# Performance work log

Hardware: AMD Instinct MI355X
Metric: run time of the kernel (lower is better)

The kernel has to match this reference:

```python
import jax, jax.numpy as jnp
import numpy as np

EMB = 1280
MD = 200
N = 20000
E = 200000
LN_EPS = 1e-5


def _layer_norm(x, g, b):
    mu = jnp.mean(x, axis=-1, keepdims=True)
    var = jnp.mean((x - mu) ** 2, axis=-1, keepdims=True)
    return (x - mu) * jax.lax.rsqrt(var + LN_EPS) * g + b


def _gat_conv(x, edge_index, edge_attr, W, We, a_src, a_dst, a_edge, bias, heads, C):
    """PyG GATConv (bias-free lin, edge_dim, add_self_loops with fill='mean')."""
    n = x.shape[0]
    src, dst = edge_index[0], edge_index[1]
    # self-loop edge_attr = mean of incoming edge_attr per dst node (0 if none)
    cnt = jax.ops.segment_sum(jnp.ones((edge_attr.shape[0],), x.dtype), dst, n)
    s = jax.ops.segment_sum(edge_attr, dst, n)
    loop_attr = jnp.where(cnt[:, None] > 0, s / jnp.maximum(cnt, 1.0)[:, None], 0.0)
    loop = jnp.arange(n)
    src = jnp.concatenate([src, loop])
    dst = jnp.concatenate([dst, loop])
    ea = jnp.concatenate([edge_attr, loop_attr], axis=0)
    h = (x @ W).reshape(n, heads, C)                      # [N,H,C]
    al_s = jnp.einsum('nhc,hc->nh', h, a_src)
    al_d = jnp.einsum('nhc,hc->nh', h, a_dst)
    eh = (ea @ We).reshape(-1, heads, C)                  # [E+N,H,C]
    al_e = jnp.einsum('ehc,hc->eh', eh, a_edge)
    alpha = jax.nn.leaky_relu(al_s[src] + al_d[dst] + al_e, 0.2)
    amax = jax.ops.segment_max(alpha, dst, n)
    amax = jnp.where(jnp.isfinite(amax), amax, 0.0)
    ex = jnp.exp(alpha - amax[dst])
    denom = jax.ops.segment_sum(ex, dst, n)
    w = ex / (denom[dst] + 1e-16)                         # segment softmax over dst
    out = jax.ops.segment_sum(h[src] * w[:, :, None], dst, n)
    return out.reshape(n, heads * C) + bias


def _forward(x, edge_index, edge_attr,
             ca_qw, ca_qb, ca_kw, ca_kb, ca_vw, ca_vb, ca_ow, ca_ob,
             g0_w, g0_ew, g0_as, g0_ad, g0_ae, g0_b, ln0_g, ln0_b,
             g1_w, g1_ew, g1_as, g1_ad, g1_ae, g1_b, ln1_g, ln1_b,
             g2_w, g2_ew, g2_as, g2_ad, g2_ae, g2_b, ln2_g, ln2_b,
             cls_w1, cls_b1, cls_w2, cls_b2):
    xe = x[:, :EMB]
    md = x[0, EMB:]
    # CrossAttention: single md vector -> K,V are [1,hidden]
    Q = xe @ ca_qw + ca_qb                                # [N,hid]
    K = md @ ca_kw + ca_kb                                # [hid]
    V = md @ ca_vw + ca_vb                                # [hid]
    scores = (Q @ K) / jnp.sqrt(jnp.asarray(Q.shape[-1], Q.dtype))  # [N]
    wts = jax.nn.softmax(scores, axis=0)[:, None]         # softmax over nodes
    attended = wts * V[None, :]                           # [N,hid]
    h = attended @ ca_ow + ca_ob + xe                     # [N,EMB]

    h = _gat_conv(h, edge_index, edge_attr, g0_w, g0_ew, g0_as, g0_ad, g0_ae, g0_b, 4, 256)
    h = jax.nn.relu(_layer_norm(h, ln0_g, ln0_b))
    h = _gat_conv(h, edge_index, edge_attr, g1_w, g1_ew, g1_as, g1_ad, g1_ae, g1_b, 4, 256)
    h = jax.nn.relu(_layer_norm(h, ln1_g, ln1_b))
    h = _gat_conv(h, edge_index, edge_attr, g2_w, g2_ew, g2_as, g2_ad, g2_ae, g2_b, 1, 256)
    h = jax.nn.relu(_layer_norm(h, ln2_g, ln2_b))

    g = jnp.mean(h, axis=0, keepdims=True)                # [1,256]
    g = jax.nn.relu(g @ cls_w1 + cls_b1)
    return g @ cls_w2 + cls_b2                            # [1,2]


def setup_inputs() -> dict:
    key = jax.random.key(0)
    ks = jax.random.split(key, 64)
    i = [0]
    def nrm(shape, scale=0.05):
        i[0] += 1
        return jax.random.normal(ks[i[0]], shape, jnp.float32) * scale
    inp = {}
    inp['x'] = nrm((N, EMB + MD), 1.0)
    inp['edge_index'] = jax.random.randint(ks[60], (2, E), 0, N, jnp.int64 if jax.config.read('jax_enable_x64') else jnp.int32)
    inp['edge_attr'] = jax.random.uniform(ks[61], (E, 1), jnp.float32)
    inp.update(ca_qw=nrm((EMB, 256)), ca_qb=jnp.zeros((256,), jnp.float32),
               ca_kw=nrm((MD, 256)), ca_kb=jnp.zeros((256,), jnp.float32),
               ca_vw=nrm((MD, 256)), ca_vb=jnp.zeros((256,), jnp.float32),
               ca_ow=nrm((256, EMB)), ca_ob=jnp.zeros((EMB,), jnp.float32))
    inp.update(g0_w=nrm((EMB, 1024)), g0_ew=nrm((1, 1024)), g0_as=nrm((4, 256)),
               g0_ad=nrm((4, 256)), g0_ae=nrm((4, 256)), g0_b=jnp.zeros((1024,), jnp.float32),
               ln0_g=jnp.ones((1024,), jnp.float32), ln0_b=jnp.zeros((1024,), jnp.float32))
    inp.update(g1_w=nrm((1024, 1024)), g1_ew=nrm((1, 1024)), g1_as=nrm((4, 256)),
               g1_ad=nrm((4, 256)), g1_ae=nrm((4, 256)), g1_b=jnp.zeros((1024,), jnp.float32),
               ln1_g=jnp.ones((1024,), jnp.float32), ln1_b=jnp.zeros((1024,), jnp.float32))
    inp.update(g2_w=nrm((1024, 256)), g2_ew=nrm((1, 256)), g2_as=nrm((1, 256)),
               g2_ad=nrm((1, 256)), g2_ae=nrm((1, 256)), g2_b=jnp.zeros((256,), jnp.float32),
               ln2_g=jnp.ones((256,), jnp.float32), ln2_b=jnp.zeros((256,), jnp.float32))
    inp.update(cls_w1=nrm((256, 128)), cls_b1=jnp.zeros((128,), jnp.float32),
               cls_w2=nrm((128, 2)), cls_b2=jnp.zeros((2,), jnp.float32))
    return inp


def reference(x, edge_index, edge_attr,
              ca_qw, ca_qb, ca_kw, ca_kb, ca_vw, ca_vb, ca_ow, ca_ob,
              g0_w, g0_ew, g0_as, g0_ad, g0_ae, g0_b, ln0_g, ln0_b,
              g1_w, g1_ew, g1_as, g1_ad, g1_ae, g1_b, ln1_g, ln1_b,
              g2_w, g2_ew, g2_as, g2_ad, g2_ae, g2_b, ln2_g, ln2_b,
              cls_w1, cls_b1, cls_w2, cls_b2):
    return _forward(x, edge_index, edge_attr,
                    ca_qw, ca_qb, ca_kw, ca_kb, ca_vw, ca_vb, ca_ow, ca_ob,
                    g0_w, g0_ew, g0_as, g0_ad, g0_ae, g0_b, ln0_g, ln0_b,
                    g1_w, g1_ew, g1_as, g1_ad, g1_ae, g1_b, ln1_g, ln1_b,
                    g2_w, g2_ew, g2_as, g2_ad, g2_ae, g2_b, ln2_g, ln2_b,
                    cls_w1, cls_b1, cls_w2, cls_b2)
```

## Files before the change

### kernel.cpp

```cpp
#include <hip/hip_runtime.h>
#include <hip/hip_bf16.h>
#include <math.h>

#define N_NODES 20000
#define N_EDGES 200000
#define XROW    1480

typedef __attribute__((ext_vector_type(8))) _Float16 f16x8;
typedef __attribute__((ext_vector_type(8))) unsigned short u16x8;
typedef __attribute__((ext_vector_type(4))) float f32x4v;

__device__ __forceinline__ float wsum(float v){
#pragma unroll
  for (int o=32;o>0;o>>=1) v += __shfl_down(v,o);
  return v;
}
__device__ __forceinline__ float wmax(float v){
#pragma unroll
  for (int o=32;o>0;o>>=1) v = fmaxf(v,__shfl_down(v,o));
  return v;
}
__device__ __forceinline__ float wsum_all(float v){
#pragma unroll
  for (int o=32;o>0;o>>=1) v += __shfl_xor(v,o);
  return v;
}
__device__ __forceinline__ float wmax_all(float v){
#pragma unroll
  for (int o=32;o>0;o>>=1) v = fmaxf(v,__shfl_xor(v,o));
  return v;
}

__device__ __forceinline__ unsigned short f2hu(float f){
  _Float16 h = (_Float16)f;
  return __builtin_bit_cast(unsigned short, h);
}
__device__ __forceinline__ float hu2f(unsigned short u){
  return (float)__builtin_bit_cast(_Float16, u);
}

__device__ __forceinline__ void async_copy16(void* lds, const void* g){
  __builtin_amdgcn_global_load_lds((const __attribute__((address_space(1))) void*)g,
                                   (__attribute__((address_space(3))) void*)lds, 16, 0, 0);
}

__global__ void edge_count_kernel(const int* __restrict__ ei, const float* __restrict__ ea,
                                  int* __restrict__ cnt, float* __restrict__ easum, int E){
  int e = blockIdx.x*256 + threadIdx.x;
  if (e >= E) return;
  int dst = ei[E + e];
  atomicAdd(&cnt[dst], 1);
  atomicAdd(&easum[dst], ea[e]);
}

__launch_bounds__(1024)
__global__ void scan_kernel(const int* __restrict__ cnt, const float* __restrict__ easum,
                            int* __restrict__ off, float* __restrict__ loop_attr, int n){
  __shared__ int buf[1024];
  const int PER = (N_NODES + 1023)/1024;
  int t = threadIdx.x;
  int base = t*PER;
  int local[PER];
  int s = 0;
#pragma unroll
  for (int k=0;k<PER;k++){
    int i = base + k;
    int v = (i<n)? cnt[i] : 0;
    local[k] = v;
    s += v;
  }
  buf[t] = s;
  __syncthreads();
  for (int d2=1; d2<1024; d2<<=1){
    int tv = (t>=d2)? buf[t-d2] : 0;
    __syncthreads();
    buf[t] += tv;
    __syncthreads();
  }
  int run = buf[t] - s;
#pragma unroll
  for (int k=0;k<PER;k++){
    int i = base + k;
    if (i < n){
      off[i] = run;
      int v = local[k];
      loop_attr[i] = (v>0) ? easum[i]/(float)v : 0.f;
      run += v;
    }
  }
  if (t == 1023) off[n] = buf[1023];
}

__global__ void edge_fill_kernel(const int* __restrict__ ei, const float* __restrict__ ea,
                                 const int* __restrict__ off, int* __restrict__ fill,
                                 int* __restrict__ csr_src, float* __restrict__ csr_ea, int E){
  int e = blockIdx.x*256 + threadIdx.x;
  if (e >= E) return;
  int dst = ei[E + e];
  int pos = off[dst] + atomicAdd(&fill[dst], 1);
  csr_src[pos] = ei[e];
  csr_ea[pos]  = ea[e];
}

__global__ void x_to_f16(const float* __restrict__ x, unsigned short* __restrict__ xh){
  const int CH4 = 1280/4;
  long total = (long)N_NODES*CH4;
  for (long i = (long)blockIdx.x*256 + threadIdx.x; i < total; i += (long)gridDim.x*256){
    int row = (int)(i / CH4), c4 = (int)(i % CH4);
    float4 v = *(const float4*)(x + (size_t)row*XROW + c4*4);
    ushort4 o;
    o.x = f2hu(v.x); o.y = f2hu(v.y); o.z = f2hu(v.z); o.w = f2hu(v.w);
    *(ushort4*)(xh + (size_t)row*1280 + c4*4) = o;
  }
}

__global__ void wt_f16_kernel(const float* __restrict__ W, int K, int N,
                              unsigned short* __restrict__ Wt){
  __shared__ float tile[32][33];
  int k0 = blockIdx.x*32, n0 = blockIdx.y*32;
  int tx = threadIdx.x & 31, ty = threadIdx.x >> 5;
  for (int r=ty; r<32; r+=8) tile[r][tx] = W[(size_t)(k0+r)*N + n0+tx];
  __syncthreads();
  for (int r=ty; r<32; r+=8){
    float w = tile[tx][r];
    Wt[(size_t)(n0+r)*K + k0+tx] = f2hu(w);
  }
}

__global__ void kv_kernel(const float* __restrict__ x,
                          const float* __restrict__ kw, const float* __restrict__ kb,
                          const float* __restrict__ vw, const float* __restrict__ vb,
                          float* __restrict__ Kv, float* __restrict__ Vv){
  int j = threadIdx.x;
  float ka = kb[j], va = vb[j];
  for (int k=0;k<200;k++){
    float m = x[1280+k];
    ka = fmaf(m, kw[k*256+j], ka);
    va = fmaf(m, vw[k*256+j], va);
  }
  Kv[j]=ka; Vv[j]=va;
}

__global__ void qkvo_kernel(const float* __restrict__ qw, const float* __restrict__ ow,
                            const float* __restrict__ Kv, const float* __restrict__ Vv,
                            float* __restrict__ qK, float* __restrict__ Vo){
  int idx = blockIdx.x*256 + threadIdx.x;
  if (idx < 1280){
    float a=0;
    for (int j=0;j<256;j++) a = fmaf(qw[idx*256+j], Kv[j], a);
    qK[idx]=a;
  } else if (idx < 2560){
    int j = idx-1280;
    float a=0;
    for (int i=0;i<256;i++) a = fmaf(Vv[i], ow[(size_t)i*1280+j], a);
    Vo[j]=a;
  }
}

__global__ void obw_kernel(const float* __restrict__ ob, const float* __restrict__ Vo,
                           const float* __restrict__ W, float* __restrict__ obW, float* __restrict__ VoW){
  int j = blockIdx.x*256 + threadIdx.x;
  float a=0,b=0;
  for (int i=0;i<1280;i++){
    float w = W[(size_t)i*1024+j];
    a = fmaf(ob[i], w, a);
    b = fmaf(Vo[i], w, b);
  }
  obW[j]=a; VoW[j]=b;
}

__launch_bounds__(256)
__global__ void scores_kernel(const unsigned short* __restrict__ xh, const float* __restrict__ qK,
                              float* __restrict__ scores, int n){
  __shared__ float qs[1280];
  int t = threadIdx.x;
  for (int i=t;i<1280;i+=256) qs[i]=qK[i];
  __syncthreads();
  int wid = t>>6, lane = t&63;
  int node = blockIdx.x*4 + wid;
  if (node >= n) return;
  const u16x8* row = (const u16x8*)(xh + (size_t)node*1280);
  float acc = 0;
#pragma unroll
  for (int it=0; it<3; it++){
    int chunk = it*64 + lane;
    if (chunk < 160){
      u16x8 v = row[chunk];
#pragma unroll
      for (int k=0;k<8;k++) acc = fmaf(hu2f(v[k]), qs[chunk*8+k], acc);
    }
  }
  acc = wsum(acc);
  if (lane==0) scores[node] = acc;
}

__launch_bounds__(1024)
__global__ void softmax_nodes(const float* __restrict__ scores, float* __restrict__ wts, int n){
  __shared__ float red[16];
  int t = threadIdx.x, lane=t&63, wid=t>>6;
  float m = -INFINITY;
  for (int i=t;i<n;i+=1024) m = fmaxf(m, scores[i]);
  m = wmax(m);
  if (lane==0) red[wid]=m;
  __syncthreads();
  if (t==0){ float r=red[0]; for (int k=1;k<16;k++) r=fmaxf(r,red[k]); red[0]=r; }
  __syncthreads();
  float M = red[0];
  __syncthreads();
  float z=0;
  for (int i=t;i<n;i+=1024) z += expf((scores[i]-M)*(1.f/16.f));
  z = wsum(z);
  if (lane==0) red[wid]=z;
  __syncthreads();
  if (t==0){ float r=0; for (int k=0;k<16;k++) r+=red[k]; red[0]=r; }
  __syncthreads();
  float invZ = 1.f/red[0];
  for (int i=t;i<n;i+=1024) wts[i] = expf((scores[i]-M)*(1.f/16.f))*invZ;
}

__launch_bounds__(256)
__global__ void gemm_f16(const unsigned short* __restrict__ A,
                         const unsigned short* __restrict__ B,
                         unsigned short* __restrict__ C, int M, int N, int K,
                         const float* __restrict__ addCol,
                         const float* __restrict__ vCol,
                         const float* __restrict__ wRow,
                         const float* __restrict__ a_src,
                         const float* __restrict__ a_dst,
                         float* __restrict__ alsp,
                         float* __restrict__ aldp)
{
  __shared__ short lds[2*2*128*64];

  const int ntc = N >> 7;
  const int sh  = __popc(ntc - 1);
  const int g   = blockIdx.y >> sh;
  const int nt  = blockIdx.y & (ntc - 1);
  const int band = blockIdx.x + (g << 3);
  if (band * 128 >= M) return;

  const int t = threadIdx.x;
  const int w = t>>6, l = t&63;
  const int bm = band*128, bn = nt*128;
  const int wr = (w>>1)*64, wc = (w&1)*64;
  const int half = w & 1;

  f32x4v acc[4][4];
#pragma unroll
  for (int i=0;i<4;i++)
#pragma unroll
    for (int j=0;j<4;j++) acc[i][j] = (f32x4v){0.f,0.f,0.f,0.f};

  const unsigned short* Ap[4]; const unsigned short* Bp[4];
  int ldsOff[4];
#pragma unroll
  for (int q=0;q<4;q++){
    int p  = (w*4+q)*64 + l;
    int r  = p>>3, pc = p&7;
    int kc = (pc ^ (r&7))*8;
    int rowA = bm + r; if (rowA > M-1) rowA = M-1;
    Ap[q] = A + (size_t)rowA*K + kc;
    Bp[q] = B + (size_t)(bn+r)*K + kc;
    ldsOff[q] = (w*4+q)*64*8;
  }

  const int nsteps = K >> 6;

#pragma unroll
  for (int q=0;q<4;q++) async_copy16(lds + ldsOff[q],        Ap[q]);
#pragma unroll
  for (int q=0;q<4;q++) async_copy16(lds + 8192 + ldsOff[q], Bp[q]);

  const int q4 = l>>4, m16 = l&15;

  for (int ks0=0; ks0<nsteps; ++ks0){
    short* curb = lds + (ks0&1)*16384;

    if (ks0+1 < nsteps){
      short* nxt = lds + ((ks0+1)&1)*16384;
      const int k0n = (ks0+1)*64;
#pragma unroll
      for (int q=0;q<4;q++) async_copy16(nxt + ldsOff[q],        Ap[q] + k0n);
#pragma unroll
      for (int q=0;q<4;q++) async_copy16(nxt + 8192 + ldsOff[q], Bp[q] + k0n);
      asm volatile("s_waitcnt vmcnt(8)" ::: "memory");
    } else {
      asm volatile("s_waitcnt vmcnt(0)" ::: "memory");
    }
    __builtin_amdgcn_sched_barrier(0);
    __builtin_amdgcn_s_barrier();
    __builtin_amdgcn_sched_barrier(0);

    __builtin_amdgcn_s_setprio(1);
#pragma unroll
    for (int ks=0; ks<2; ks++){
      f16x8 af[4], bf[4];
      const int c = ks*4 + q4;
#pragma unroll
      for (int i=0;i<4;i++){
        int ra = wr + i*16 + m16;
        af[i] = *(const f16x8*)&curb[ra*64 + ((c ^ (ra&7))*8)];
        int rb = wc + i*16 + m16;
        bf[i] = *(const f16x8*)&curb[8192 + rb*64 + ((c ^ (rb&7))*8)];
      }
#pragma unroll
      for (int i=0;i<4;i++)
#pragma unroll
        for (int j=0;j<4;j++)
          acc[i][j] = __builtin_amdgcn_mfma_f32_16x16x32_f16(af[i], bf[j], acc[i][j], 0,0,0);
    }
    __builtin_amdgcn_s_setprio(0);
    __builtin_amdgcn_sched_barrier(0);
    __builtin_amdgcn_s_barrier();
    __builtin_amdgcn_sched_barrier(0);
  }

  float* sred = (float*)lds;
  float* dred = sred + 256;
  float asv[4], adv[4];
#pragma unroll
  for (int j=0;j<4;j++){
    int n = bn + wc + j*16 + m16;
    asv[j] = a_src[n];
    adv[j] = a_dst[n];
  }
#pragma unroll
  for (int i=0;i<4;i++){
#pragma unroll
    for (int r=0;r<4;r++){
      int rloc = wr + i*16 + q4*4 + r;
      int m = bm + rloc;
      float wrow = addCol ? wRow[m < M ? m : M-1] : 0.f;
      float vj[4];
#pragma unroll
      for (int j=0;j<4;j++){
        int n = bn + wc + j*16 + m16;
        float v = acc[i][j][r];
        if (addCol) v += addCol[n] + wrow*vCol[n];
        vj[j] = v;
      }
      if (m < M){
        unsigned short* crow = C + (size_t)m*N;
#pragma unroll
        for (int j=0;j<4;j++) crow[bn + wc + j*16 + m16] = f2hu(vj[j]);
      }
      float s = vj[0]*asv[0] + vj[1]*asv[1] + vj[2]*asv[2] + vj[3]*asv[3];
      float d = vj[0]*adv[0] + vj[1]*adv[1] + vj[2]*adv[2] + vj[3]*adv[3];
#pragma unroll
      for (int o=1;o<16;o<<=1){ s += __shfl_xor(s,o); d += __shfl_xor(d,o); }
      if (m16 == 0){
        sred[half*128 + rloc] = s;
        dred[half*128 + rloc] = d;
      }
    }
  }
  __syncthreads();
  if (t < 128){
    int m = bm + t;
    if (m < M){
      alsp[(size_t)nt*M + m] = sred[t] + sred[128+t];
      aldp[(size_t)nt*M + m] = dred[t] + dred[128+t];
    }
  }
}

__global__ void als_combine(const float* __restrict__ alsp, const float* __restrict__ aldp,
                            float* __restrict__ als, float* __restrict__ ald, int M, int H){
  int idx = blockIdx.x*256 + threadIdx.x;
  if (idx >= M*H) return;
  int m = idx / H, hh = idx - m*H;
  als[idx] = alsp[(size_t)(2*hh)*M + m] + alsp[(size_t)(2*hh+1)*M + m];
  ald[idx] = aldp[(size_t)(2*hh)*M + m] + aldp[(size_t)(2*hh+1)*M + m];
}

template<int H>
__global__ void we_kernel(const float* __restrict__ We, const float* __restrict__ a_edge,
                          float* __restrict__ we){
  int wid = threadIdx.x>>6, lane = threadIdx.x&63;
  if (wid < H){
    const float4* w4 = (const float4*)(We + wid*256);
    const float4* a4 = (const float4*)(a_edge + wid*256);
    float4 a = w4[lane], b = a4[lane];
    float v = a.x*b.x + a.y*b.y + a.z*b.z + a.w*b.w;
    v = wsum(v);
    if (lane==0) we[wid]=v;
  }
}

template<int H>
__launch_bounds__(256)
__global__ void gat_agg_ln_wave(const unsigned short* __restrict__ hmat,
                           const float* __restrict__ als, const float* __restrict__ ald,
                           const int* __restrict__ off, const int* __restrict__ csr_src,
                           const float* __restrict__ csr_ea, const float* __restrict__ loop_attr,
                           const float* __restrict__ we,
                           const float* __restrict__ bias,
                           const float* __restrict__ ln_g, const float* __restrict__ ln_b,
                           float* __restrict__ outf, unsigned short* __restrict__ outb, int n)
{
  constexpr int OUT = 256*H;
  constexpr int CPL = OUT/64;
  const int wv = threadIdx.x>>6, lane = threadIdx.x&63;
  const int i = blockIdx.x*4 + wv;
  __shared__ float wbuf_s[4][64*H];
  __shared__ int   sbuf_s[4][64];
  if (i >= n) return;
  float* wbuf = wbuf_s[wv];
  int*   sbuf = sbuf_s[wv];

  const int begin = off[i];
  const int deg   = off[i+1]-begin;
  const int S     = deg + 1;

  float aldi[H], wei[H];
#pragma unroll
  for (int hh=0;hh<H;hh++){ aldi[hh]=ald[(size_t)i*H+hh]; wei[hh]=we[hh]; }
  const float lea = loop_attr[i];

  const int head = (lane*CPL) >> 8;
  const int c0   = lane*CPL;
  float acc[CPL];
#pragma unroll
  for (int c=0;c<CPL;c++) acc[c]=0.f;

  if (S <= 64){
    int src = i; float ev = lea;
    if (lane < deg){ src = csr_src[begin+lane]; ev = csr_ea[begin+lane]; }
    const bool act = lane < S;
    float a[H];
#pragma unroll
    for (int hh=0;hh<H;hh++){
      float v = als[(size_t)src*H+hh] + aldi[hh] + ev*wei[hh];
      a[hh] = v>0.f ? v : 0.2f*v;
    }
#pragma unroll
    for (int hh=0;hh<H;hh++){
      float M = wmax_all(act ? a[hh] : -INFINITY);
      float e = act ? __expf(a[hh]-M) : 0.f;
      float Z = wsum_all(e);
      wbuf[lane*H+hh] = e / (Z + 1e-16f);
    }
    sbuf[lane] = src;
    for (int j=0;j<S;j++){
      int sj = sbuf[j];
      float wj = wbuf[j*H+head];
      const unsigned short* row = hmat + (size_t)sj*OUT + c0;
      if constexpr (CPL==16){
        u16x8 r0 = *(const u16x8*)(row);
        u16x8 r1 = *(const u16x8*)(row+8);
#pragma unroll
        for (int c=0;c<8;c++){
          acc[c]   = fmaf(wj, hu2f(r0[c]), acc[c]);
          acc[8+c] = fmaf(wj, hu2f(r1[c]), acc[8+c]);
        }
      } else {
        ushort4 r = *(const ushort4*)(row);
        acc[0]=fmaf(wj,hu2f(r.x),acc[0]); acc[1]=fmaf(wj,hu2f(r.y),acc[1]);
        acc[2]=fmaf(wj,hu2f(r.z),acc[2]); acc[3]=fmaf(wj,hu2f(r.w),acc[3]);
      }
    }
  } else {
    float rm[H];
#pragma unroll
    for (int hh=0;hh<H;hh++) rm[hh] = -INFINITY;
    for (int s=lane; s<S; s+=64){
      int src = (s<deg)? csr_src[begin+s] : i;
      float ev = (s<deg)? csr_ea[begin+s] : lea;
#pragma unroll
      for (int hh=0;hh<H;hh++){
        float v = als[(size_t)src*H+hh] + aldi[hh] + ev*wei[hh];
        v = v>0.f? v : 0.2f*v;
        rm[hh] = fmaxf(rm[hh], v);
      }
    }
    float M[H], es[H];
#pragma unroll
    for (int hh=0;hh<H;hh++){ M[hh]=wmax_all(rm[hh]); es[hh]=0.f; }
    for (int s=lane; s<S; s+=64){
      int src = (s<deg)? csr_src[begin+s] : i;
      float ev = (s<deg)? csr_ea[begin+s] : lea;
#pragma unroll
      for (int hh=0;hh<H;hh++){
        float v = als[(size_t)src*H+hh] + aldi[hh] + ev*wei[hh];
        v = v>0.f? v : 0.2f*v;
        es[hh] += __expf(v - M[hh]);
      }
    }
    float invZ[H];
#pragma unroll
    for (int hh=0;hh<H;hh++) invZ[hh] = 1.f/(wsum_all(es[hh]) + 1e-16f);
    for (int cb=0; cb<S; cb+=64){
      int m = min(64, S-cb);
      int s = cb + lane;
      if (s < S){
        int src = (s<deg)? csr_src[begin+s] : i;
        float ev = (s<deg)? csr_ea[begin+s] : lea;
        sbuf[lane] = src;
#pragma unroll
        for (int hh=0;hh<H;hh++){
          float v = als[(size_t)src*H+hh] + aldi[hh] + ev*wei[hh];
          v = v>0.f? v : 0.2f*v;
          wbuf[lane*H+hh] = __expf(v - M[hh]) * invZ[hh];
        }
      }
      for (int j=0;j<m;j++){
        int sj = sbuf[j];
        float wj = wbuf[j*H+head];
        const unsigned short* row = hmat + (size_t)sj*OUT + c0;
        if constexpr (CPL==16){
          u16x8 r0 = *(const u16x8*)(row);
          u16x8 r1 = *(const u16x8*)(row+8);
#pragma unroll
          for (int c=0;c<8;c++){
            acc[c]   = fmaf(wj, hu2f(r0[c]), acc[c]);
            acc[8+c] = fmaf(wj, hu2f(r1[c]), acc[8+c]);
          }
        } else {
          ushort4 r = *(const ushort4*)(row);
          acc[0]=fmaf(wj,hu2f(r.x),acc[0]); acc[1]=fmaf(wj,hu2f(r.y),acc[1]);
          acc[2]=fmaf(wj,hu2f(r.z),acc[2]); acc[3]=fmaf(wj,hu2f(r.w),acc[3]);
        }
      }
    }
  }

  float vals[CPL];
  float ls=0.f;
#pragma unroll
  for (int c=0;c<CPL;c+=4){
    float4 b4 = *(const float4*)(bias + c0 + c);
    vals[c]=acc[c]+b4.x; vals[c+1]=acc[c+1]+b4.y; vals[c+2]=acc[c+2]+b4.z; vals[c+3]=acc[c+3]+b4.w;
    ls += vals[c]+vals[c+1]+vals[c+2]+vals[c+3];
  }
  float mu = wsum_all(ls) * (1.f/OUT);
  float lv=0.f;
#pragma unroll
  for (int c=0;c<CPL;c++){ float d=vals[c]-mu; lv += d*d; }
  float inv = rsqrtf(wsum_all(lv)*(1.f/OUT) + 1e-5f);

  if (outb){
    if constexpr (CPL==16){
#pragma unroll
      for (int c=0;c<CPL;c+=8){
        u16x8 o;
#pragma unroll
        for (int k=0;k<8;k++){
          float g = ln_g[c0+c+k], b = ln_b[c0+c+k];
          o[k] = f2hu(fmaxf((vals[c+k]-mu)*inv*g + b, 0.f));
        }
        *(u16x8*)(outb + (size_t)i*OUT + c0 + c) = o;
      }
    } else {
      ushort4 o;
      o.x = f2hu(fmaxf((vals[0]-mu)*inv*ln_g[c0+0] + ln_b[c0+0], 0.f));
      o.y = f2hu(fmaxf((vals[1]-mu)*inv*ln_g[c0+1] + ln_b[c0+1], 0.f));
      o.z = f2hu(fmaxf((vals[2]-mu)*inv*ln_g[c0+2] + ln_b[c0+2], 0.f));
      o.w = f2hu(fmaxf((vals[3]-mu)*inv*ln_g[c0+3] + ln_b[c0+3], 0.f));
      *(ushort4*)(outb + (size_t)i*OUT + c0) = o;
    }
  } else {
#pragma unroll
    for (int c=0;c<CPL;c+=4){
      float4 g4 = *(const float4*)(ln_g + c0 + c);
      float4 b4 = *(const float4*)(ln_b + c0 + c);
      float4 o;
      o.x = fmaxf((vals[c+0]-mu)*inv*g4.x + b4.x, 0.f);
      o.y = fmaxf((vals[c+1]-mu)*inv*g4.y + b4.y, 0.f);
      o.z = fmaxf((vals[c+2]-mu)*inv*g4.z + b4.z, 0.f);
      o.w = fmaxf((vals[c+3]-mu)*inv*g4.w + b4.w, 0.f);
      *(float4*)(outf + (size_t)i*OUT + c0 + c) = o;
    }
  }
}

__global__ void colsum_kernel(const float* __restrict__ h2, float* __restrict__ gsum, int n){
  int c = threadIdx.x;
  float acc=0;
  for (int i=blockIdx.x;i<n;i+=gridDim.x) acc += h2[(size_t)i*256 + c];
  atomicAdd(&gsum[c], acc);
}

__launch_bounds__(128)
__global__ void cls_kernel(const float* __restrict__ gsum,
                           const float* __restrict__ w1, const float* __restrict__ b1,
                           const float* __restrict__ w2, const float* __restrict__ b2,
                           float* __restrict__ outp){
  __shared__ float g[256];
  __shared__ float hid[128];
  int t = threadIdx.x;
  g[t]     = gsum[t]    *(1.f/N_NODES);
  g[t+128] = gsum[t+128]*(1.f/N_NODES);
  __syncthreads();
  float a = b1[t];
  for (int c=0;c<256;c++) a = fmaf(g[c], w1[c*128+t], a);
  hid[t] = fmaxf(a, 0.f);
  __syncthreads();
  if (t<2){
    float o = b2[t];
    for (int j=0;j<128;j++) o = fmaf(hid[j], w2[j*2+t], o);
    outp[t] = o;
  }
}

extern "C" void kernel_launch(void* const* d_in, const int* in_sizes, int n_in,
                              void* d_out, int out_size, void* d_ws, size_t ws_size,
                              hipStream_t stream)
{
  const float* x      = (const float*)d_in[0];
  const int*   ei     = (const int*)  d_in[1];
  const float* ea     = (const float*)d_in[2];
  const float* ca_qw  = (const float*)d_in[3];
  const float* ca_kw  = (const float*)d_in[5];
  const float* ca_kb  = (const float*)d_in[6];
  const float* ca_vw  = (const float*)d_in[7];
  const float* ca_vb  = (const float*)d_in[8];
  const float* ca_ow  = (const float*)d_in[9];
  const float* ca_ob  = (const float*)d_in[10];
  const float* g0_w   = (const float*)d_in[11];
  const float* g0_ew  = (const float*)d_in[12];
  const float* g0_as  = (const float*)d_in[13];
  const float* g0_ad  = (const float*)d_in[14];
  const float* g0_ae  = (const float*)d_in[15];
  const float* g0_b   = (const float*)d_in[16];
  const float* ln0_g  = (const float*)d_in[17];
  const float* ln0_b  = (const float*)d_in[18];
  const float* g1_w   = (const float*)d_in[19];
  const float* g1_ew  = (const float*)d_in[20];
  const float* g1_as  = (const float*)d_in[21];
  const float* g1_ad  = (const float*)d_in[22];
  const float* g1_ae  = (const float*)d_in[23];
  const float* g1_b   = (const float*)d_in[24];
  const float* ln1_g  = (const float*)d_in[25];
  const float* ln1_b  = (const float*)d_in[26];
  const float* g2_w   = (const float*)d_in[27];
  const float* g2_ew  = (const float*)d_in[28];
  const float* g2_as  = (const float*)d_in[29];
  const float* g2_ad  = (const float*)d_in[30];
  const float* g2_ae  = (const float*)d_in[31];
  const float* g2_b   = (const float*)d_in[32];
  const float* ln2_g  = (const float*)d_in[33];
  const float* ln2_b  = (const float*)d_in[34];
  const float* cls_w1 = (const float*)d_in[35];
  const float* cls_b1 = (const float*)d_in[36];
  const float* cls_w2 = (const float*)d_in[37];
  const float* cls_b2 = (const float*)d_in[38];
  float* outp = (float*)d_out;

  const int N = N_NODES, E = N_EDGES;

  char* base = (char*)d_ws;
  size_t o = 0;
  auto alloc = [&](size_t bytes)->void*{
    void* p = base + o;
    o += (bytes + 255) & ~(size_t)255;
    return p;
  };
  unsigned short* hF   = (unsigned short*)alloc((size_t)N*1024*2);
  unsigned short* Af   = (unsigned short*)alloc((size_t)N*1280*2);
  float*          h2   = (float*)         alloc((size_t)N*256*4);
  unsigned short* Wt   = (unsigned short*)alloc((size_t)1280*1024*2);
  float* alsp      = (float*)alloc((size_t)8*N*4);
  float* aldp      = (float*)alloc((size_t)8*N*4);
  float* als       = (float*)alloc((size_t)2*N*4*4);
  float* ald       = als + (size_t)N*4;
  float* scores    = (float*)alloc((size_t)N*4);
  float* wts       = (float*)alloc((size_t)N*4);
  int*   cnt       = (int*)  alloc((size_t)N*4);
  float* easum     = (float*)alloc((size_t)N*4);
  int*   off       = (int*)  alloc((size_t)(N+1)*4);
  int*   fill      = (int*)  alloc((size_t)N*4);
  int*   csr_src   = (int*)  alloc((size_t)E*4);
  float* csr_ea    = (float*)alloc((size_t)E*4);
  float* loop_attr = (float*)alloc((size_t)N*4);
  float* Kv        = (float*)alloc(256*4);
  float* Vv        = (float*)alloc(256*4);
  float* qK        = (float*)alloc(1280*4);
  float* Vo        = (float*)alloc(1280*4);
  float* obW       = (float*)alloc(1024*4);
  float* VoW       = (float*)alloc(1024*4);
  float* web       = (float*)alloc(16*4);
  float* gsum      = (float*)alloc(256*4);

  hipMemsetAsync(cnt,   0, (size_t)N*4, stream);
  hipMemsetAsync(easum, 0, (size_t)N*4, stream);
  hipMemsetAsync(fill,  0, (size_t)N*4, stream);
  hipMemsetAsync(gsum,  0, 256*4,       stream);

  int eblocks = (E + 255)/256;
  edge_count_kernel<<<eblocks,256,0,stream>>>(ei, ea, cnt, easum, E);
  scan_kernel<<<1,1024,0,stream>>>(cnt, easum, off, loop_attr, N);
  edge_fill_kernel<<<eblocks,256,0,stream>>>(ei, ea, off, fill, csr_src, csr_ea, E);

  x_to_f16<<<2048,256,0,stream>>>(x, Af);

  kv_kernel<<<1,256,0,stream>>>(x, ca_kw, ca_kb, ca_vw, ca_vb, Kv, Vv);
  qkvo_kernel<<<10,256,0,stream>>>(ca_qw, ca_ow, Kv, Vv, qK, Vo);
  obw_kernel<<<4,256,0,stream>>>(ca_ob, Vo, g0_w, obW, VoW);
  scores_kernel<<<(N+3)/4,256,0,stream>>>(Af, qK, scores, N);
  softmax_nodes<<<1,1024,0,stream>>>(scores, wts, N);

  const int mTiles  = (N + 127)/128;
  const int mGroups = (mTiles + 7)/8;
  const int NB4 = (N + 3)/4;

  wt_f16_kernel<<<dim3(1280/32, 1024/32),256,0,stream>>>(g0_w, 1280, 1024, Wt);
  gemm_f16<<<dim3(8, mGroups*8),256,0,stream>>>(Af, Wt, hF, N, 1024, 1280, obW, VoW, wts,
                                                g0_as, g0_ad, alsp, aldp);
  als_combine<<<(N*4+255)/256,256,0,stream>>>(alsp, aldp, als, ald, N, 4);
  we_kernel<4><<<1,256,0,stream>>>(g0_ew, g0_ae, web);
  gat_agg_ln_wave<4><<<NB4,256,0,stream>>>(hF, als, ald, off, csr_src, csr_ea, loop_attr,
                                           web, g0_b, ln0_g, ln0_b, nullptr, Af, N);

  wt_f16_kernel<<<dim3(1024/32, 1024/32),256,0,stream>>>(g1_w, 1024, 1024, Wt);
  gemm_f16<<<dim3(8, mGroups*8),256,0,stream>>>(Af, Wt, hF, N, 1024, 1024, nullptr, nullptr, nullptr,
                                                g1_as, g1_ad, alsp, aldp);
  als_combine<<<(N*4+255)/256,256,0,stream>>>(alsp, aldp, als, ald, N, 4);
  we_kernel<4><<<1,256,0,stream>>>(g1_ew, g1_ae, web);
  gat_agg_ln_wave<4><<<NB4,256,0,stream>>>(hF, als, ald, off, csr_src, csr_ea, loop_attr,
                                           web, g1_b, ln1_g, ln1_b, nullptr, Af, N);

  wt_f16_kernel<<<dim3(1024/32, 256/32),256,0,stream>>>(g2_w, 1024, 256, Wt);
  gemm_f16<<<dim3(8, mGroups*2),256,0,stream>>>(Af, Wt, hF, N, 256, 1024, nullptr, nullptr, nullptr,
                                                g2_as, g2_ad, alsp, aldp);
  als_combine<<<(N+255)/256,256,0,stream>>>(alsp, aldp, als, ald, N, 1);
  we_kernel<1><<<1,256,0,stream>>>(g2_ew, g2_ae, web);
  gat_agg_ln_wave<1><<<NB4,256,0,stream>>>(hF, als, ald, off, csr_src, csr_ea, loop_attr,
                                           web, g2_b, ln2_g, ln2_b, h2, nullptr, N);

  colsum_kernel<<<256,256,0,stream>>>(h2, gsum, N);
  cls_kernel<<<1,128,0,stream>>>(gsum, cls_w1, cls_b1, cls_w2, cls_b2, outp);

  (void)in_sizes; (void)n_in; (void)out_size; (void)ws_size;
}
```

Before: 862.6 us.

## Fuse f16 conversion with scores, merge we into als_combine, prefetch gather rows

```diff
diff --git a/kernel.cpp b/kernel.cpp
--- a/kernel.cpp
+++ b/kernel.cpp
@@ -100,18 +100,6 @@
   int pos = off[dst] + atomicAdd(&fill[dst], 1);
   csr_src[pos] = ei[e];
   csr_ea[pos]  = ea[e];
-}
-
-__global__ void x_to_f16(const float* __restrict__ x, unsigned short* __restrict__ xh){
-  const int CH4 = 1280/4;
-  long total = (long)N_NODES*CH4;
-  for (long i = (long)blockIdx.x*256 + threadIdx.x; i < total; i += (long)gridDim.x*256){
-    int row = (int)(i / CH4), c4 = (int)(i % CH4);
-    float4 v = *(const float4*)(x + (size_t)row*XROW + c4*4);
-    ushort4 o;
-    o.x = f2hu(v.x); o.y = f2hu(v.y); o.z = f2hu(v.z); o.w = f2hu(v.w);
-    *(ushort4*)(xh + (size_t)row*1280 + c4*4) = o;
-  }
 }
 
 __global__ void wt_f16_kernel(const float* __restrict__ W, int K, int N,
@@ -170,8 +158,8 @@
 }
 
 __launch_bounds__(256)
-__global__ void scores_kernel(const unsigned short* __restrict__ xh, const float* __restrict__ qK,
-                              float* __restrict__ scores, int n){
+__global__ void xh_scores_kernel(const float* __restrict__ x, const float* __restrict__ qK,
+                                 unsigned short* __restrict__ xh, float* __restrict__ scores, int n){
   __shared__ float qs[1280];
   int t = threadIdx.x;
   for (int i=t;i<1280;i+=256) qs[i]=qK[i];
@@ -179,16 +167,20 @@
   int wid = t>>6, lane = t&63;
   int node = blockIdx.x*4 + wid;
   if (node >= n) return;
-  const u16x8* row = (const u16x8*)(xh + (size_t)node*1280);
-  float acc = 0;
-#pragma unroll
-  for (int it=0; it<3; it++){
-    int chunk = it*64 + lane;
-    if (chunk < 160){
-      u16x8 v = row[chunk];
-#pragma unroll
-      for (int k=0;k<8;k++) acc = fmaf(hu2f(v[k]), qs[chunk*8+k], acc);
-    }
+  const float* xr = x + (size_t)node*XROW;
+  unsigned short* orow = xh + (size_t)node*1280;
+  float acc = 0.f;
+#pragma unroll
+  for (int it=0; it<5; it++){
+    int c4 = it*64 + lane;
+    float4 v = *(const float4*)(xr + c4*4);
+    ushort4 o;
+    o.x = f2hu(v.x); o.y = f2hu(v.y); o.z = f2hu(v.z); o.w = f2hu(v.w);
+    *(ushort4*)(orow + c4*4) = o;
+    acc = fmaf(v.x, qs[c4*4+0], acc);
+    acc = fmaf(v.y, qs[c4*4+1], acc);
+    acc = fmaf(v.z, qs[c4*4+2], acc);
+    acc = fmaf(v.w, qs[c4*4+3], acc);
   }
   acc = wsum(acc);
   if (lane==0) scores[node] = acc;
@@ -208,14 +200,14 @@
   float M = red[0];
   __syncthreads();
   float z=0;
-  for (int i=t;i<n;i+=1024) z += expf((scores[i]-M)*(1.f/16.f));
+  for (int i=t;i<n;i+=1024) z += __expf((scores[i]-M)*(1.f/16.f));
   z = wsum(z);
   if (lane==0) red[wid]=z;
   __syncthreads();
   if (t==0){ float r=0; for (int k=0;k<16;k++) r+=red[k]; red[0]=r; }
   __syncthreads();
   float invZ = 1.f/red[0];
-  for (int i=t;i<n;i+=1024) wts[i] = expf((scores[i]-M)*(1.f/16.f))*invZ;
+  for (int i=t;i<n;i+=1024) wts[i] = __expf((scores[i]-M)*(1.f/16.f))*invZ;
 }
 
 __launch_bounds__(256)
@@ -365,26 +357,25 @@
 }
 
 __global__ void als_combine(const float* __restrict__ alsp, const float* __restrict__ aldp,
-                            float* __restrict__ als, float* __restrict__ ald, int M, int H){
+                            float* __restrict__ als, float* __restrict__ ald, int M, int H,
+                            const float* __restrict__ We, const float* __restrict__ a_edge,
+                            float* __restrict__ we){
+  if (blockIdx.x == 0){
+    int wid = threadIdx.x>>6, lane = threadIdx.x&63;
+    if (wid < H){
+      const float4* w4 = (const float4*)(We + wid*256);
+      const float4* a4 = (const float4*)(a_edge + wid*256);
+      float4 a = w4[lane], b = a4[lane];
+      float v = a.x*b.x + a.y*b.y + a.z*b.z + a.w*b.w;
+      v = wsum(v);
+      if (lane==0) we[wid]=v;
+    }
+  }
   int idx = blockIdx.x*256 + threadIdx.x;
   if (idx >= M*H) return;
   int m = idx / H, hh = idx - m*H;
   als[idx] = alsp[(size_t)(2*hh)*M + m] + alsp[(size_t)(2*hh+1)*M + m];
   ald[idx] = aldp[(size_t)(2*hh)*M + m] + aldp[(size_t)(2*hh+1)*M + m];
-}
-
-template<int H>
-__global__ void we_kernel(const float* __restrict__ We, const float* __restrict__ a_edge,
-                          float* __restrict__ we){
-  int wid = threadIdx.x>>6, lane = threadIdx.x&63;
-  if (wid < H){
-    const float4* w4 = (const float4*)(We + wid*256);
-    const float4* a4 = (const float4*)(a_edge + wid*256);
-    float4 a = w4[lane], b = a4[lane];
-    float v = a.x*b.x + a.y*b.y + a.z*b.z + a.w*b.w;
-    v = wsum(v);
-    if (lane==0) we[wid]=v;
-  }
 }
 
 template<int H>
@@ -427,36 +418,115 @@
     int src = i; float ev = lea;
     if (lane < deg){ src = csr_src[begin+lane]; ev = csr_ea[begin+lane]; }
     const bool act = lane < S;
-    float a[H];
-#pragma unroll
-    for (int hh=0;hh<H;hh++){
-      float v = als[(size_t)src*H+hh] + aldi[hh] + ev*wei[hh];
-      a[hh] = v>0.f ? v : 0.2f*v;
-    }
-#pragma unroll
-    for (int hh=0;hh<H;hh++){
-      float M = wmax_all(act ? a[hh] : -INFINITY);
-      float e = act ? __expf(a[hh]-M) : 0.f;
-      float Z = wsum_all(e);
-      wbuf[lane*H+hh] = e / (Z + 1e-16f);
-    }
     sbuf[lane] = src;
-    for (int j=0;j<S;j++){
-      int sj = sbuf[j];
-      float wj = wbuf[j*H+head];
-      const unsigned short* row = hmat + (size_t)sj*OUT + c0;
-      if constexpr (CPL==16){
-        u16x8 r0 = *(const u16x8*)(row);
-        u16x8 r1 = *(const u16x8*)(row+8);
+
+    if constexpr (CPL==16){
+      u16x8 a0r0,a0r1,a1r0,a1r1;
+      {
+        const unsigned short* r0p = hmat + (size_t)sbuf[0]*OUT + c0;
+        a0r0 = *(const u16x8*)r0p; a0r1 = *(const u16x8*)(r0p+8);
+        a1r0 = a0r0; a1r1 = a0r1;
+        if (S > 1){
+          const unsigned short* r1p = hmat + (size_t)sbuf[1]*OUT + c0;
+          a1r0 = *(const u16x8*)r1p; a1r1 = *(const u16x8*)(r1p+8);
+        }
+      }
+      float a[H];
+#pragma unroll
+      for (int hh=0;hh<H;hh++){
+        float v = als[(size_t)src*H+hh] + aldi[hh] + ev*wei[hh];
+        a[hh] = v>0.f ? v : 0.2f*v;
+      }
+#pragma unroll
+      for (int hh=0;hh<H;hh++){
+        float M = wmax_all(act ? a[hh] : -INFINITY);
+        float e = act ? __expf(a[hh]-M) : 0.f;
+        float Z = wsum_all(e);
+        wbuf[lane*H+hh] = e / (Z + 1e-16f);
+      }
+      int j = 0;
+      for (; j+2<S; j+=2){
+        u16x8 n0r0,n0r1,n1r0,n1r1;
+        {
+          const unsigned short* rp = hmat + (size_t)sbuf[j+2]*OUT + c0;
+          n0r0 = *(const u16x8*)rp; n0r1 = *(const u16x8*)(rp+8);
+          n1r0 = n0r0; n1r1 = n0r1;
+          if (j+3 < S){
+            const unsigned short* rq = hmat + (size_t)sbuf[j+3]*OUT + c0;
+            n1r0 = *(const u16x8*)rq; n1r1 = *(const u16x8*)(rq+8);
+          }
+        }
+        float w0 = wbuf[j*H+head], w1 = wbuf[(j+1)*H+head];
 #pragma unroll
         for (int c=0;c<8;c++){
-          acc[c]   = fmaf(wj, hu2f(r0[c]), acc[c]);
-          acc[8+c] = fmaf(wj, hu2f(r1[c]), acc[8+c]);
-        }
-      } else {
-        ushort4 r = *(const ushort4*)(row);
-        acc[0]=fmaf(wj,hu2f(r.x),acc[0]); acc[1]=fmaf(wj,hu2f(r.y),acc[1]);
-        acc[2]=fmaf(wj,hu2f(r.z),acc[2]); acc[3]=fmaf(wj,hu2f(r.w),acc[3]);
+          acc[c]   = fmaf(w0, hu2f(a0r0[c]), acc[c]);
+          acc[8+c] = fmaf(w0, hu2f(a0r1[c]), acc[8+c]);
+        }
+#pragma unroll
+        for (int c=0;c<8;c++){
+          acc[c]   = fmaf(w1, hu2f(a1r0[c]), acc[c]);
+          acc[8+c] = fmaf(w1, hu2f(a1r1[c]), acc[8+c]);
+        }
+        a0r0=n0r0; a0r1=n0r1; a1r0=n1r0; a1r1=n1r1;
+      }
+      {
+        float w0 = wbuf[j*H+head];
+#pragma unroll
+        for (int c=0;c<8;c++){
+          acc[c]   = fmaf(w0, hu2f(a0r0[c]), acc[c]);
+          acc[8+c] = fmaf(w0, hu2f(a0r1[c]), acc[8+c]);
+        }
+        if (j+1 < S){
+          float w1 = wbuf[(j+1)*H+head];
+#pragma unroll
+          for (int c=0;c<8;c++){
+            acc[c]   = fmaf(w1, hu2f(a1r0[c]), acc[c]);
+            acc[8+c] = fmaf(w1, hu2f(a1r1[c]), acc[8+c]);
+          }
+        }
+      }
+    } else {
+      ushort4 a0, a1;
+      {
+        a0 = *(const ushort4*)(hmat + (size_t)sbuf[0]*OUT + c0);
+        a1 = a0;
+        if (S > 1) a1 = *(const ushort4*)(hmat + (size_t)sbuf[1]*OUT + c0);
+      }
+      float a[H];
+#pragma unroll
+      for (int hh=0;hh<H;hh++){
+        float v = als[(size_t)src*H+hh] + aldi[hh] + ev*wei[hh];
+        a[hh] = v>0.f ? v : 0.2f*v;
+      }
+#pragma unroll
+      for (int hh=0;hh<H;hh++){
+        float M = wmax_all(act ? a[hh] : -INFINITY);
+        float e = act ? __expf(a[hh]-M) : 0.f;
+        float Z = wsum_all(e);
+        wbuf[lane*H+hh] = e / (Z + 1e-16f);
+      }
+      int j = 0;
+      for (; j+2<S; j+=2){
+        ushort4 n0, n1;
+        n0 = *(const ushort4*)(hmat + (size_t)sbuf[j+2]*OUT + c0);
+        n1 = n0;
+        if (j+3 < S) n1 = *(const ushort4*)(hmat + (size_t)sbuf[j+3]*OUT + c0);
+        float w0 = wbuf[j*H+head], w1 = wbuf[(j+1)*H+head];
+        acc[0]=fmaf(w0,hu2f(a0.x),acc[0]); acc[1]=fmaf(w0,hu2f(a0.y),acc[1]);
+        acc[2]=fmaf(w0,hu2f(a0.z),acc[2]); acc[3]=fmaf(w0,hu2f(a0.w),acc[3]);
+        acc[0]=fmaf(w1,hu2f(a1.x),acc[0]); acc[1]=fmaf(w1,hu2f(a1.y),acc[1]);
+        acc[2]=fmaf(w1,hu2f(a1.z),acc[2]); acc[3]=fmaf(w1,hu2f(a1.w),acc[3]);
+        a0=n0; a1=n1;
+      }
+      {
+        float w0 = wbuf[j*H+head];
+        acc[0]=fmaf(w0,hu2f(a0.x),acc[0]); acc[1]=fmaf(w0,hu2f(a0.y),acc[1]);
+        acc[2]=fmaf(w0,hu2f(a0.z),acc[2]); acc[3]=fmaf(w0,hu2f(a0.w),acc[3]);
+        if (j+1 < S){
+          float w1 = wbuf[(j+1)*H+head];
+          acc[0]=fmaf(w1,hu2f(a1.x),acc[0]); acc[1]=fmaf(w1,hu2f(a1.y),acc[1]);
+          acc[2]=fmaf(w1,hu2f(a1.z),acc[2]); acc[3]=fmaf(w1,hu2f(a1.w),acc[3]);
+        }
       }
     }
   } else {
@@ -691,12 +761,10 @@
   scan_kernel<<<1,1024,0,stream>>>(cnt, easum, off, loop_attr, N);
   edge_fill_kernel<<<eblocks,256,0,stream>>>(ei, ea, off, fill, csr_src, csr_ea, E);
 
-  x_to_f16<<<2048,256,0,stream>>>(x, Af);
-
   kv_kernel<<<1,256,0,stream>>>(x, ca_kw, ca_kb, ca_vw, ca_vb, Kv, Vv);
   qkvo_kernel<<<10,256,0,stream>>>(ca_qw, ca_ow, Kv, Vv, qK, Vo);
+  xh_scores_kernel<<<(N+3)/4,256,0,stream>>>(x, qK, Af, scores, N);
   obw_kernel<<<4,256,0,stream>>>(ca_ob, Vo, g0_w, obW, VoW);
-  scores_kernel<<<(N+3)/4,256,0,stream>>>(Af, qK, scores, N);
   softmax_nodes<<<1,1024,0,stream>>>(scores, wts, N);
 
   const int mTiles  = (N + 127)/128;
@@ -706,24 +774,21 @@
   wt_f16_kernel<<<dim3(1280/32, 1024/32),256,0,stream>>>(g0_w, 1280, 1024, Wt);
   gemm_f16<<<dim3(8, mGroups*8),256,0,stream>>>(Af, Wt, hF, N, 1024, 1280, obW, VoW, wts,
                                                 g0_as, g0_ad, alsp, aldp);
-  als_combine<<<(N*4+255)/256,256,0,stream>>>(alsp, aldp, als, ald, N, 4);
-  we_kernel<4><<<1,256,0,stream>>>(g0_ew, g0_ae, web);
+  als_combine<<<(N*4+255)/256,256,0,stream>>>(alsp, aldp, als, ald, N, 4, g0_ew, g0_ae, web);
   gat_agg_ln_wave<4><<<NB4,256,0,stream>>>(hF, als, ald, off, csr_src, csr_ea, loop_attr,
                                            web, g0_b, ln0_g, ln0_b, nullptr, Af, N);
 
   wt_f16_kernel<<<dim3(1024/32, 1024/32),256,0,stream>>>(g1_w, 1024, 1024, Wt);
   gemm_f16<<<dim3(8, mGroups*8),256,0,stream>>>(Af, Wt, hF, N, 1024, 1024, nullptr, nullptr, nullptr,
                                                 g1_as, g1_ad, alsp, aldp);
-  als_combine<<<(N*4+255)/256,256,0,stream>>>(alsp, aldp, als, ald, N, 4);
-  we_kernel<4><<<1,256,0,stream>>>(g1_ew, g1_ae, web);
+  als_combine<<<(N*4+255)/256,256,0,stream>>>(alsp, aldp, als, ald, N, 4, g1_ew, g1_ae, web);
   gat_agg_ln_wave<4><<<NB4,256,0,stream>>>(hF, als, ald, off, csr_src, csr_ea, loop_attr,
                                            web, g1_b, ln1_g, ln1_b, nullptr, Af, N);
 
   wt_f16_kernel<<<dim3(1024/32, 256/32),256,0,stream>>>(g2_w, 1024, 256, Wt);
   gemm_f16<<<dim3(8, mGroups*2),256,0,stream>>>(Af, Wt, hF, N, 256, 1024, nullptr, nullptr, nullptr,
                                                 g2_as, g2_ad, alsp, aldp);
-  als_combine<<<(N+255)/256,256,0,stream>>>(alsp, aldp, als, ald, N, 1);
-  we_kernel<1><<<1,256,0,stream>>>(g2_ew, g2_ae, web);
+  als_combine<<<(N+255)/256,256,0,stream>>>(alsp, aldp, als, ald, N, 1, g2_ew, g2_ae, web);
   gat_agg_ln_wave<1><<<NB4,256,0,stream>>>(hF, als, ald, off, csr_src, csr_ea, loop_attr,
                                            web, g2_b, ln2_g, ln2_b, h2, nullptr, N);
 
```

Result: no change. 855.9 us (-0.8%).
